# Performance work log

Measured on AMD Instinct MI355X. Metric: run time of the kernel, lower is better.

The kernel has to match this reference:

```python
import jax, jax.numpy as jnp
import numpy as np

N = 6720      # 16 graphs * 420 nodes
E = 33600     # 16 graphs * 2100 edges (5 per node)
DIN = 2048
H1, C1 = 2, 1024   # conv1: heads=2, out=1024 -> concat 2048
H2, C2 = 1, 64     # conv2: heads=1, out=64
ED = 64            # edge_dim
NODES_PER_GRAPH = 420


def _lin(k, fi, fo):
    return jax.random.normal(k, (fi, fo), jnp.float32) / np.sqrt(fi).astype(np.float32)


def setup_inputs() -> dict:
    key = jax.random.key(0)
    ks = jax.random.split(key, 24)
    d = {}
    d["x"] = jax.random.normal(ks[0], (N, DIN), jnp.float32)
    d["edge_index"] = jax.random.randint(ks[1], (2, E), 0, N)
    # tiled learned edge_features param (torch.rand init), one 2100xED block per graph
    ef = jax.random.uniform(ks[2], (5 * NODES_PER_GRAPH, ED), jnp.float32)
    d["edge_attr"] = jnp.tile(ef, (N // NODES_PER_GRAPH, 1))
    HC1 = H1 * C1
    d["q1_w"] = _lin(ks[3], DIN, HC1); d["q1_b"] = jax.random.normal(ks[4], (HC1,)) * 0.01
    d["k1_w"] = _lin(ks[5], DIN, HC1); d["k1_b"] = jax.random.normal(ks[6], (HC1,)) * 0.01
    d["v1_w"] = _lin(ks[7], DIN, HC1); d["v1_b"] = jax.random.normal(ks[8], (HC1,)) * 0.01
    d["e1_w"] = _lin(ks[9], ED, HC1)                      # lin_edge has no bias in PyG
    d["s1_w"] = _lin(ks[10], DIN, HC1); d["s1_b"] = jax.random.normal(ks[11], (HC1,)) * 0.01
    HC2 = H2 * C2
    d["q2_w"] = _lin(ks[12], HC1, HC2); d["q2_b"] = jax.random.normal(ks[13], (HC2,)) * 0.01
    d["k2_w"] = _lin(ks[14], HC1, HC2); d["k2_b"] = jax.random.normal(ks[15], (HC2,)) * 0.01
    d["v2_w"] = _lin(ks[16], HC1, HC2); d["v2_b"] = jax.random.normal(ks[17], (HC2,)) * 0.01
    d["e2_w"] = _lin(ks[18], ED, HC2)
    d["s2_w"] = _lin(ks[19], HC1, HC2); d["s2_b"] = jax.random.normal(ks[20], (HC2,)) * 0.01
    return d


def _transformer_conv(x, src, dst, edge_attr, qw, qb, kw, kb, vw, vb, ew, sw, sb, H, C):
    """PyG TransformerConv (concat=True, beta=False, root_weight=True)."""
    n = x.shape[0]
    q = (x @ qw + qb).reshape(n, H, C)
    k = (x @ kw + kb).reshape(n, H, C)
    v = (x @ vw + vb).reshape(n, H, C)
    e = (edge_attr @ ew).reshape(-1, H, C)         # [E,H,C]
    kj = k[src] + e                                # gather source keys + edge emb
    alpha = jnp.sum(q[dst] * kj, axis=-1) / np.sqrt(C).astype(np.float32)  # [E,H]
    # scatter-softmax over incoming edges of each target node
    amax = jax.ops.segment_max(alpha, dst, num_segments=n)   # [N,H]
    ex = jnp.exp(alpha - amax[dst])
    denom = jax.ops.segment_sum(ex, dst, num_segments=n)
    attn = ex / (denom[dst] + 1e-16)               # [E,H]
    msg = (v[src] + e) * attn[..., None]           # [E,H,C]
    out = jax.ops.segment_sum(msg, dst, num_segments=n).reshape(n, H * C)
    return out + x @ sw + sb                       # root/skip connection


def reference(x, edge_index, edge_attr,
              q1_w, q1_b, k1_w, k1_b, v1_w, v1_b, e1_w, s1_w, s1_b,
              q2_w, q2_b, k2_w, k2_b, v2_w, v2_b, e2_w, s2_w, s2_b):
    src, dst = edge_index[0], edge_index[1]
    h = jax.nn.relu(_transformer_conv(x, src, dst, edge_attr,
                                      q1_w, q1_b, k1_w, k1_b, v1_w, v1_b,
                                      e1_w, s1_w, s1_b, H1, C1))
    h = jax.nn.relu(_transformer_conv(h, src, dst, edge_attr,
                                      q2_w, q2_b, k2_w, k2_b, v2_w, v2_b,
                                      e2_w, s2_w, s2_b, H2, C2))
    return h.reshape(-1, NODES_PER_GRAPH * 64)     # forward returns here (fc layers are dead code)
```

## Files before the change

### kernel.cpp

```cpp
#include <hip/hip_runtime.h>
#include <hip/hip_bf16.h>
#include <cstdint>
#include <cstddef>

#define NN    6720
#define MPAD  6912
#define NE    33600
#define KDIM  2048
#define HC1   2048
#define EAP   2100

typedef __attribute__((ext_vector_type(8))) short bhalf8;
typedef __attribute__((ext_vector_type(4))) short bhalf4;
typedef __attribute__((ext_vector_type(4))) float fx4;

__device__ __forceinline__ float bf2f(short s) {
    union { unsigned int u; float f; } c;
    c.u = ((unsigned int)(unsigned short)s) << 16;
    return c.f;
}

__device__ __forceinline__ void gload16(const __hip_bfloat16* g, void* lds)
{
    __builtin_amdgcn_global_load_lds(
        (const __attribute__((address_space(1))) unsigned int*)g,
        (__attribute__((address_space(3))) unsigned int*)lds,
        16, 0, 0);
}

#define CFENCE asm volatile("" ::: "memory")

__global__ __launch_bounds__(256, 2) void gemm256x128_fused(
    const __hip_bfloat16* __restrict__ A,
    const __hip_bfloat16* __restrict__ Bt,
    const float* __restrict__ bcat,
    __hip_bfloat16* __restrict__ oq,
    __hip_bfloat16* __restrict__ ok,
    __hip_bfloat16* __restrict__ ov,
    __hip_bfloat16* __restrict__ oh)
{
    __shared__ alignas(16) char Lds[73728];

    const int bid = blockIdx.x;
    const int i0  = bid >> 3;
    const int bx  = (bid & 7) * 8 + (i0 & 7);
    const int by  = i0 >> 3;

    const int tid  = threadIdx.x;
    const int w    = tid >> 6;
    const int lane = tid & 63;
    const int wm = w >> 1, wn = w & 1;
    const int rowA = by * 256;
    const int rowB = bx * 128;

    const int sug = ((lane & 3) ^ ((lane >> 3) & 3)) << 3;
    const __hip_bfloat16* Ag0 = A  + (size_t)(rowA + w * 64 + (lane >> 2)) * KDIM + sug;
    const __hip_bfloat16* Bg0 = Bt + (size_t)(rowB + w * 32 + (lane >> 2)) * KDIM + sug;

    const int rds = (((lane >> 4) ^ (((lane & 15) >> 1) & 3)) << 4);

    fx4 acc[8][4] = {};

#define STAGE(T)                                                          \
    { const int s_ = (T) % 3; const int k0_ = (T) * 32;                   \
      char* ab_ = Lds + s_ * 16384 + w * 4096;                            \
      char* bb_ = Lds + 49152 + s_ * 8192 + w * 2048;                     \
      gload16(Ag0 + k0_, ab_);                                            \
      gload16(Ag0 + k0_ + 16 * KDIM, ab_ + 1024);                         \
      gload16(Ag0 + k0_ + 32 * KDIM, ab_ + 2048);                         \
      gload16(Ag0 + k0_ + 48 * KDIM, ab_ + 3072);                         \
      gload16(Bg0 + k0_, bb_);                                            \
      gload16(Bg0 + k0_ + 16 * KDIM, bb_ + 1024); }

#define TILE(T, VM, DOSTAGE)                                              \
    { if (DOSTAGE) { STAGE((T) + 2); }                                    \
      asm volatile("s_waitcnt vmcnt(" VM ")" ::: "memory");               \
      __builtin_amdgcn_s_barrier(); CFENCE;                               \
      const int s_ = (T) % 3;                                             \
      const char* ap_ = Lds + s_ * 16384;                                 \
      const char* bp_ = Lds + 49152 + s_ * 8192;                          \
      bhalf8 af_[8], bf_[4];                                              \
      _Pragma("unroll")                                                   \
      for (int nj = 0; nj < 4; ++nj)                                      \
          bf_[nj] = *(const bhalf8*)(bp_ + (wn * 64 + nj * 16 + (lane & 15)) * 64 + rds); \
      _Pragma("unroll")                                                   \
      for (int mi = 0; mi < 8; ++mi)                                      \
          af_[mi] = *(const bhalf8*)(ap_ + (wm * 128 + mi * 16 + (lane & 15)) * 64 + rds); \
      __builtin_amdgcn_s_setprio(1);                                      \
      _Pragma("unroll")                                                   \
      for (int mi = 0; mi < 8; ++mi)                                      \
          _Pragma("unroll")                                               \
          for (int nj = 0; nj < 4; ++nj)                                  \
              acc[mi][nj] = __builtin_amdgcn_mfma_f32_16x16x32_bf16(      \
                  af_[mi], bf_[nj], acc[mi][nj], 0, 0, 0);                \
      __builtin_amdgcn_s_setprio(0); CFENCE;                              \
      __builtin_amdgcn_s_barrier(); CFENCE; }

    STAGE(0); STAGE(1);
    for (int t = 0; t < (KDIM / 32) - 2; ++t) {
        TILE(t, "12", 1);
    }
    TILE((KDIM / 32) - 2, "6", 0);
    TILE((KDIM / 32) - 1, "0", 0);

#undef TILE
#undef STAGE

    const int gcol = rowB + wn * 64;
    const int seg  = gcol >> 11;
    const int lcol = gcol & 2047;
    float bv[4];
    #pragma unroll
    for (int nj = 0; nj < 4; ++nj) bv[nj] = bcat[gcol + nj * 16 + (lane & 15)];
    char* scr = Lds + w * 8704;
    const int growA = rowA + wm * 128;
    __hip_bfloat16* dst = (seg == 0) ? oq : (seg == 1) ? ok : (seg == 2) ? ov : oh;

    #pragma unroll
    for (int c = 0; c < 4; ++c) {
        #pragma unroll
        for (int m2 = 0; m2 < 2; ++m2) {
            const int mi = c * 2 + m2;
            #pragma unroll
            for (int nj = 0; nj < 4; ++nj) {
                const int cl = nj * 16 + (lane & 15);
                #pragma unroll
                for (int i2 = 0; i2 < 4; ++i2) {
                    const int rl = m2 * 16 + ((lane >> 4) << 2) + i2;
                    *(float*)(scr + rl * 272 + cl * 4) = acc[mi][nj][i2] + bv[nj];
                }
            }
        }
        asm volatile("s_waitcnt lgkmcnt(0)" ::: "memory");
        CFENCE;
        const int rrow = (lane >> 4);
        const int u    = lane & 15;
        #pragma unroll
        for (int p = 0; p < 8; ++p) {
            const int row = p * 4 + rrow;
            const float4 f = *(const float4*)(scr + row * 272 + u * 16);
            bhalf4 tb;
            tb[0] = (short)__bfloat16_as_ushort(__float2bfloat16(f.x));
            tb[1] = (short)__bfloat16_as_ushort(__float2bfloat16(f.y));
            tb[2] = (short)__bfloat16_as_ushort(__float2bfloat16(f.z));
            tb[3] = (short)__bfloat16_as_ushort(__float2bfloat16(f.w));
            *(bhalf4*)&dst[(size_t)(growA + c * 32 + row) * 2048 + lcol + u * 4] = tb;
        }
        asm volatile("s_waitcnt lgkmcnt(0)" ::: "memory");
        CFENCE;
    }
}

__global__ __launch_bounds__(256) void gemm_bf16(
    const __hip_bfloat16* __restrict__ A,
    const __hip_bfloat16* __restrict__ Bt,
    const float* __restrict__ bias,
    float* __restrict__ C,
    __hip_bfloat16* __restrict__ Cb,
    int M, int N, int K, int flags)
{
    __shared__ alignas(16) __hip_bfloat16 Asm[128 * 64];
    __shared__ alignas(16) __hip_bfloat16 Bsm[128 * 64];
    const int tid  = threadIdx.x;
    const int w    = tid >> 6;
    const int lane = tid & 63;
    const int wr = w >> 1, wc = w & 1;
    const int rowA = blockIdx.y * 128;
    const int rowB = blockIdx.x * 128;
    const int klen = K / gridDim.z;
    const int kbeg = blockIdx.z * klen;

    const int srow = w * 32 + (lane >> 3);
    const int ug8  = ((lane & 7) ^ (lane >> 3)) << 3;
    const __hip_bfloat16* Ag = A  + (size_t)(rowA + srow) * K + ug8;
    const __hip_bfloat16* Bg = Bt + (size_t)(rowB + srow) * K + ug8;
    char* AsBase = (char*)Asm + w * 4096;
    char* BsBase = (char*)Bsm + w * 4096;

    fx4 acc[4][4] = {};

    const int fra = wr * 64 + (lane & 15);
    const int frb = wc * 64 + (lane & 15);
    const int kb  = (lane >> 4) << 4;
    const int swz = (lane & 7) << 4;

    for (int k0 = kbeg; k0 < kbeg + klen; k0 += 64) {
        __syncthreads();
        #pragma unroll
        for (int j = 0; j < 4; ++j) {
            gload16(Ag + (size_t)j * 8 * K + k0, AsBase + j * 1024);
            gload16(Bg + (size_t)j * 8 * K + k0, BsBase + j * 1024);
        }
        __syncthreads();
        #pragma unroll
        for (int kk = 0; kk < 2; ++kk) {
            const int cb = kk * 64 + kb;
            bhalf8 af[4], bfr[4];
            #pragma unroll
            for (int mi = 0; mi < 4; ++mi)
                af[mi] = *(const bhalf8*)((const char*)Asm + (fra + mi * 16) * 128 + (cb ^ swz));
            #pragma unroll
            for (int nj = 0; nj < 4; ++nj)
                bfr[nj] = *(const bhalf8*)((const char*)Bsm + (frb + nj * 16) * 128 + (cb ^ swz));
            #pragma unroll
            for (int mi = 0; mi < 4; ++mi)
                #pragma unroll
                for (int nj = 0; nj < 4; ++nj)
                    acc[mi][nj] = __builtin_amdgcn_mfma_f32_16x16x32_bf16(
                        af[mi], bfr[nj], acc[mi][nj], 0, 0, 0);
        }
    }

    float* Cz = C ? C + (size_t)blockIdx.z * ((size_t)M * N) : nullptr;
    #pragma unroll
    for (int nj = 0; nj < 4; ++nj) {
        const int ccol = rowB + wc * 64 + nj * 16 + (lane & 15);
        const float bv = (flags & 1) ? bias[ccol] : 0.f;
        #pragma unroll
        for (int mi = 0; mi < 4; ++mi) {
            const int crow0 = rowA + wr * 64 + mi * 16 + ((lane >> 4) << 2);
            #pragma unroll
            for (int i = 0; i < 4; ++i) {
                size_t idx = (size_t)(crow0 + i) * N + ccol;
                float v = acc[mi][nj][i] + bv;
                if (flags & 2)  v += Cz[idx];
                if (flags & 16) v += __bfloat162float(Cb[idx]);
                if (flags & 4)  v = fmaxf(v, 0.f);
                if (Cz && !(flags & 8)) Cz[idx] = v;
                if (Cb) Cb[idx] = __float2bfloat16(v);
            }
        }
    }
}

__global__ void reduce4(const float* __restrict__ parts, size_t stride,
                        const float* __restrict__ bias, int colmask,
                        float* __restrict__ dst, int n)
{
    int i = blockIdx.x * 256 + threadIdx.x;
    if (i >= n) return;
    float v = parts[i] + parts[stride + i] + parts[2 * stride + i] + parts[3 * stride + i];
    if (bias) v += bias[i & colmask];
    dst[i] = v;
}

__global__ __launch_bounds__(256) void gemm_tile(
    const float* __restrict__ A, const float* __restrict__ B,
    const float* __restrict__ bias, float* __restrict__ C,
    int M, int N, int K, int flags)
{
    __shared__ float As[16][68];
    __shared__ float Bs[16][64];
    const int tid = threadIdx.x;
    const int bx = blockIdx.x, by = blockIdx.y;
    const int tx = tid & 15, ty = tid >> 4;
    const int arow = tid >> 2, acol = (tid & 3) << 2;
    const int brow = tid >> 4, bcol = (tid & 15) << 2;
    const float* Ag = A + (size_t)(by * 64 + arow) * K + acol;
    const float* Bg = B + (size_t)brow * N + bx * 64 + bcol;
    float acc[4][4] = {};
    for (int k0 = 0; k0 < K; k0 += 16) {
        const float4 av = *(const float4*)(Ag + k0);
        const float4 bv = *(const float4*)(Bg + (size_t)k0 * N);
        __syncthreads();
        As[acol + 0][arow] = av.x;
        As[acol + 1][arow] = av.y;
        As[acol + 2][arow] = av.z;
        As[acol + 3][arow] = av.w;
        *(float4*)&Bs[brow][bcol] = bv;
        __syncthreads();
        #pragma unroll
        for (int kk = 0; kk < 16; ++kk) {
            const float4 a4 = *(const float4*)&As[kk][ty << 2];
            const float4 b4 = *(const float4*)&Bs[kk][tx << 2];
            const float a[4] = {a4.x, a4.y, a4.z, a4.w};
            const float b[4] = {b4.x, b4.y, b4.z, b4.w};
            #pragma unroll
            for (int i = 0; i < 4; ++i)
                #pragma unroll
                for (int j = 0; j < 4; ++j)
                    acc[i][j] += a[i] * b[j];
        }
    }
    const int crow = by * 64 + (ty << 2);
    const int ccol = bx * 64 + (tx << 2);
    float4 b4 = make_float4(0.f, 0.f, 0.f, 0.f);
    if (flags & 1) b4 = *(const float4*)(bias + ccol);
    #pragma unroll
    for (int i = 0; i < 4; ++i) {
        float* cp = C + (size_t)(crow + i) * N + ccol;
        float4 v;
        v.x = acc[i][0] + b4.x; v.y = acc[i][1] + b4.y;
        v.z = acc[i][2] + b4.z; v.w = acc[i][3] + b4.w;
        if (flags & 2) {
            const float4 o = *(const float4*)cp;
            v.x += o.x; v.y += o.y; v.z += o.z; v.w += o.w;
        }
        *(float4*)cp = v;
    }
}

__global__ void count_deg(const int* __restrict__ ei, int* __restrict__ deg)
{
    int e = blockIdx.x * 256 + threadIdx.x;
    if (e < NE) atomicAdd(&deg[ei[NE + e]], 1);
}

__global__ __launch_bounds__(1024) void scan_kernel(const int* __restrict__ deg,
                                                    int* __restrict__ rowptr)
{
    __shared__ int s[1024];
    const int t = threadIdx.x;
    const int base = t * 7;
    int loc[7];
    int sum = 0;
    #pragma unroll
    for (int i = 0; i < 7; ++i) {
        int idx = base + i;
        int v = (idx < NN) ? deg[idx] : 0;
        loc[i] = v; sum += v;
    }
    s[t] = sum;
    __syncthreads();
    for (int off = 1; off < 1024; off <<= 1) {
        int v = (t >= off) ? s[t - off] : 0;
        __syncthreads();
        s[t] += v;
        __syncthreads();
    }
    int running = s[t] - sum;
    #pragma unroll
    for (int i = 0; i < 7; ++i) {
        int idx = base + i;
        if (idx <= NN) rowptr[idx] = running;
        if (idx < NN) running += loc[i];
    }
}

__global__ void fill_csr(const int* __restrict__ ei, const int* __restrict__ rowptr,
                         int* __restrict__ fillctr, int* __restrict__ elist)
{
    int e = blockIdx.x * 256 + threadIdx.x;
    if (e >= NE) return;
    int d = ei[NE + e];
    int pos = atomicAdd(&fillctr[d], 1);
    elist[rowptr[d] + pos] = e;
}

__global__ void sort_csr(const int* __restrict__ rowptr, int* __restrict__ elist)
{
    int n = blockIdx.x * 256 + threadIdx.x;
    if (n >= NN) return;
    int s0 = rowptr[n], s1 = rowptr[n + 1];
    for (int i = s0 + 1; i < s1; ++i) {
        int v = elist[i];
        int j = i - 1;
        while (j >= s0 && elist[j] > v) { elist[j + 1] = elist[j]; --j; }
        elist[j + 1] = v;
    }
}

__global__ void cvt_pad_bf16(const float* __restrict__ src, __hip_bfloat16* __restrict__ dst,
                             int relu)
{
    size_t i = (size_t)(blockIdx.x * 256 + threadIdx.x) * 4;
    int row = (int)(i >> 11);
    float4 v = make_float4(0.f, 0.f, 0.f, 0.f);
    if (row < NN) v = *(const float4*)&src[i];
    if (relu) {
        v.x = fmaxf(v.x, 0.f); v.y = fmaxf(v.y, 0.f);
        v.z = fmaxf(v.z, 0.f); v.w = fmaxf(v.w, 0.f);
    }
    dst[i + 0] = __float2bfloat16(v.x);
    dst[i + 1] = __float2bfloat16(v.y);
    dst[i + 2] = __float2bfloat16(v.z);
    dst[i + 3] = __float2bfloat16(v.w);
}

__global__ __launch_bounds__(256) void transpose_cvt4(
    const float* __restrict__ W0, const float* __restrict__ W1,
    const float* __restrict__ W2, const float* __restrict__ W3,
    __hip_bfloat16* __restrict__ dst)
{
    const float* W = (blockIdx.z == 0) ? W0 : (blockIdx.z == 1) ? W1
                   : (blockIdx.z == 2) ? W2 : W3;
    __hip_bfloat16* Bt = dst + (size_t)blockIdx.z * KDIM * KDIM;
    __shared__ float t[32][33];
    int kb = blockIdx.y * 32, nb = blockIdx.x * 32;
    int tx = threadIdx.x & 31, ty = threadIdx.x >> 5;
    #pragma unroll
    for (int i = 0; i < 32; i += 8)
        t[ty + i][tx] = W[(size_t)(kb + ty + i) * KDIM + nb + tx];
    __syncthreads();
    #pragma unroll
    for (int i = 0; i < 32; i += 8)
        Bt[(size_t)(nb + ty + i) * KDIM + kb + tx] = __float2bfloat16(t[tx][ty + i]);
}

__global__ void build_misc(
    const float* __restrict__ q1b, const float* __restrict__ k1b,
    const float* __restrict__ v1b, const float* __restrict__ s1b,
    const float* __restrict__ e1w,
    const float* __restrict__ q2w, const float* __restrict__ k2w,
    const float* __restrict__ v2w, const float* __restrict__ s2w,
    const float* __restrict__ q2bb, const float* __restrict__ k2bb,
    const float* __restrict__ v2bb, const float* __restrict__ s2bb,
    float* __restrict__ bcat, __hip_bfloat16* __restrict__ w1pp,
    __hip_bfloat16* __restrict__ w1ppT, __hip_bfloat16* __restrict__ w2t,
    float* __restrict__ b2)
{
    int idx = blockIdx.x * 256 + threadIdx.x;
    if (idx < 8192) {
        int seg = idx >> 11, j = idx & 2047;
        const float* b = (seg == 0) ? q1b : (seg == 1) ? k1b : (seg == 2) ? v1b : s1b;
        bcat[idx] = b[j];
        return;
    }
    idx -= 8192;
    if (idx < 262144) {
        int p = idx >> 11, j = idx & 2047;
        float v = ((j >> 10) == (p >> 6)) ? e1w[(size_t)(p & 63) * KDIM + j] : 0.f;
        w1pp[idx] = __float2bfloat16(v);
        return;
    }
    idx -= 262144;
    if (idx < 262144) {
        int n = idx >> 7, k = idx & 127;
        float v = ((n >> 10) == (k >> 6)) ? e1w[(size_t)(k & 63) * KDIM + n] : 0.f;
        w1ppT[idx] = __float2bfloat16(v);
        return;
    }
    idx -= 262144;
    int c = idx >> 11, d = idx & 2047;
    int g = c >> 6, j = c & 63;
    const float* w = (g == 0) ? q2w : (g == 1) ? k2w : (g == 2) ? v2w : s2w;
    w2t[idx] = __float2bfloat16(w[(size_t)d * 64 + j]);
    if (d == 0) {
        const float* b = (g == 0) ? q2bb : (g == 1) ? k2bb : (g == 2) ? v2bb : s2bb;
        b2[c] = b[j];
    }
}

__global__ __launch_bounds__(256) void node1_kernel(
    const __hip_bfloat16* __restrict__ q1b, const __hip_bfloat16* __restrict__ k1b,
    const __hip_bfloat16* __restrict__ v1b,
    const float* __restrict__ P1, const float* __restrict__ ea,
    const int* __restrict__ ei, const int* __restrict__ rowptr,
    const int* __restrict__ elist,
    __hip_bfloat16* __restrict__ h1, __hip_bfloat16* __restrict__ R1)
{
    __shared__ int   s_src[256];
    __shared__ int   s_em[256];
    __shared__ float s_at[256][2];
    const int n = blockIdx.x;
    const int s0 = rowptr[n];
    const int deg = rowptr[n + 1] - s0;
    const int w = threadIdx.x >> 6, lane = threadIdx.x & 63;

    for (int j = w; j < deg; j += 4) {
        const int e = elist[s0 + j];
        const int src = ei[e];
        const int em = e % EAP;
        if (lane == 0) { s_src[j] = src; s_em[j] = em; }
        const float eaj = ea[(size_t)em * 64 + lane];
        #pragma unroll
        for (int h = 0; h < 2; ++h) {
            const __hip_bfloat16* qh = q1b + (size_t)n * HC1 + h * 1024 + lane * 16;
            const __hip_bfloat16* kh = k1b + (size_t)src * HC1 + h * 1024 + lane * 16;
            bhalf8 qa = *(const bhalf8*)qh, qc = *(const bhalf8*)(qh + 8);
            bhalf8 ka = *(const bhalf8*)kh, kc = *(const bhalf8*)(kh + 8);
            float s = 0.f;
            #pragma unroll
            for (int jj = 0; jj < 8; ++jj) s += bf2f(qa[jj]) * bf2f(ka[jj]);
            #pragma unroll
            for (int jj = 0; jj < 8; ++jj) s += bf2f(qc[jj]) * bf2f(kc[jj]);
            s += eaj * P1[(size_t)n * 128 + h * 64 + lane];
            #pragma unroll
            for (int off = 32; off; off >>= 1) s += __shfl_xor(s, off);
            if (lane == 0) s_at[j][h] = s * 0.03125f;
        }
    }
    __syncthreads();

    if (threadIdx.x < 2) {
        const int h = threadIdx.x;
        float m = -1e30f;
        for (int j = 0; j < deg; ++j) m = fmaxf(m, s_at[j][h]);
        float sum = 0.f;
        for (int j = 0; j < deg; ++j) {
            float ex = __expf(s_at[j][h] - m);
            s_at[j][h] = ex; sum += ex;
        }
        float inv = 1.f / (sum + 1e-16f);
        for (int j = 0; j < deg; ++j) s_at[j][h] *= inv;
    }
    __syncthreads();

    if (threadIdx.x < 128) {
        const int h = threadIdx.x >> 6, jj = threadIdx.x & 63;
        float r = 0.f;
        for (int j = 0; j < deg; ++j)
            r += s_at[j][h] * ea[(size_t)s_em[j] * 64 + jj];
        R1[(size_t)n * 128 + threadIdx.x] = __float2bfloat16(r);
    }

    const int c0 = threadIdx.x * 8;
    const int h = c0 >> 10;
    float acc[8];
    const bhalf8 cur = *(const bhalf8*)&h1[(size_t)n * HC1 + c0];
    #pragma unroll
    for (int jj = 0; jj < 8; ++jj) acc[jj] = bf2f(cur[jj]);
    for (int j = 0; j < deg; ++j) {
        const float at = s_at[j][h];
        bhalf8 v = *(const bhalf8*)&v1b[(size_t)s_src[j] * HC1 + c0];
        #pragma unroll
        for (int jj = 0; jj < 8; ++jj) acc[jj] += at * bf2f(v[jj]);
    }
    bhalf8 o;
    #pragma unroll
    for (int jj = 0; jj < 8; ++jj)
        o[jj] = (short)__bfloat16_as_ushort(__float2bfloat16(acc[jj]));
    *(bhalf8*)&h1[(size_t)n * HC1 + c0] = o;
}

__global__ __launch_bounds__(64) void node2_kernel(
    const float* __restrict__ qkvs2, const float* __restrict__ E2s,
    const int* __restrict__ ei, const int* __restrict__ rowptr,
    const int* __restrict__ elist, float* __restrict__ out)
{
    __shared__ float s_at[256];
    __shared__ int   s_src[256];
    __shared__ int   s_em[256];
    const int n = blockIdx.x;
    const int s0 = rowptr[n];
    const int deg = rowptr[n + 1] - s0;
    const int c = threadIdx.x;
    const float q = qkvs2[(size_t)n * 256 + c];

    for (int j = 0; j < deg; ++j) {
        const int e = elist[s0 + j];
        const int src = ei[e];
        const int em = e % EAP;
        float s = q * (qkvs2[(size_t)src * 256 + 64 + c] + E2s[(size_t)em * 64 + c]);
        #pragma unroll
        for (int off = 32; off; off >>= 1) s += __shfl_xor(s, off);
        if (c == 0) { s_at[j] = s * 0.125f; s_src[j] = src; s_em[j] = em; }
    }
    __syncthreads();
    float m = -1e30f;
    for (int j = 0; j < deg; ++j) m = fmaxf(m, s_at[j]);
    float sum = 0.f;
    for (int j = 0; j < deg; ++j) sum += __expf(s_at[j] - m);
    const float inv = 1.f / (sum + 1e-16f);

    float acc = qkvs2[(size_t)n * 256 + 192 + c];
    for (int j = 0; j < deg; ++j) {
        const float at = __expf(s_at[j] - m) * inv;
        acc += at * (qkvs2[(size_t)s_src[j] * 256 + 128 + c] + E2s[(size_t)s_em[j] * 64 + c]);
    }
    out[(size_t)n * 64 + c] = fmaxf(acc, 0.f);
}

extern "C" void kernel_launch(void* const* d_in, const int* in_sizes, int n_in,
                              void* d_out, int out_size, void* d_ws, size_t ws_size,
                              hipStream_t stream)
{
    const float* x   = (const float*)d_in[0];
    const int*   ei  = (const int*)d_in[1];
    const float* ea  = (const float*)d_in[2];
    const float* q1w = (const float*)d_in[3];
    const float* q1b = (const float*)d_in[4];
    const float* k1w = (const float*)d_in[5];
    const float* k1b = (const float*)d_in[6];
    const float* v1w = (const float*)d_in[7];
    const float* v1b = (const float*)d_in[8];
    const float* e1w = (const float*)d_in[9];
    const float* s1w = (const float*)d_in[10];
    const float* s1b = (const float*)d_in[11];
    const float* q2w = (const float*)d_in[12];
    const float* q2b = (const float*)d_in[13];
    const float* k2w = (const float*)d_in[14];
    const float* k2b = (const float*)d_in[15];
    const float* v2w = (const float*)d_in[16];
    const float* v2b = (const float*)d_in[17];
    const float* e2w = (const float*)d_in[18];
    const float* s2w = (const float*)d_in[19];
    const float* s2b = (const float*)d_in[20];
    float* out = (float*)d_out;

    char* base = (char*)d_ws;
    size_t off = 0;
    auto alloc = [&](size_t nbytes) {
        size_t o = off; off += (nbytes + 255) & ~(size_t)255; return o;
    };
    const size_t xb_off   = alloc((size_t)MPAD * KDIM * 2);
    const size_t wcat_off = alloc((size_t)4 * KDIM * KDIM * 2);
    __hip_bfloat16* xb    = (__hip_bfloat16*)(base + xb_off);
    __hip_bfloat16* wcat  = (__hip_bfloat16*)(base + wcat_off);
    float*          Cpart = (float*)(base + wcat_off);

    __hip_bfloat16* q1bb  = (__hip_bfloat16*)(base + alloc((size_t)MPAD * HC1 * 2));
    __hip_bfloat16* k1bb  = (__hip_bfloat16*)(base + alloc((size_t)MPAD * HC1 * 2));
    __hip_bfloat16* v1bb  = (__hip_bfloat16*)(base + alloc((size_t)MPAD * HC1 * 2));
    __hip_bfloat16* h1bf  = (__hip_bfloat16*)(base + alloc((size_t)MPAD * HC1 * 2));
    float*          bcat  = (float*)(base + alloc((size_t)4 * KDIM * 4));
    float*          P1    = (float*)(base + alloc((size_t)MPAD * 128 * 4));
    __hip_bfloat16* R1b   = (__hip_bfloat16*)(base + alloc((size_t)MPAD * 128 * 2));
    __hip_bfloat16* w1pp  = (__hip_bfloat16*)(base + alloc((size_t)128 * KDIM * 2));
    __hip_bfloat16* w1ppT = (__hip_bfloat16*)(base + alloc((size_t)KDIM * 128 * 2));
    __hip_bfloat16* w2t   = (__hip_bfloat16*)(base + alloc((size_t)256 * KDIM * 2));
    float*          b2    = (float*)(base + alloc(256 * 4));
    float*          qkvs2 = (float*)(base + alloc((size_t)MPAD * 256 * 4));
    float*          E2s   = (float*)(base + alloc((size_t)2112 * 64 * 4));
    int* deg    = (int*)(base + alloc((size_t)NN * 4));
    int* fill   = (int*)(base + alloc((size_t)NN * 4));
    int* rowptr = (int*)(base + alloc((size_t)(NN + 1) * 4));
    int* elist  = (int*)(base + alloc((size_t)NE * 4));

    hipMemsetAsync(deg, 0, sizeof(int) * 2 * NN, stream);
    count_deg<<<(NE + 255) / 256, 256, 0, stream>>>(ei, deg);
    scan_kernel<<<1, 1024, 0, stream>>>(deg, rowptr);
    fill_csr<<<(NE + 255) / 256, 256, 0, stream>>>(ei, rowptr, fill, elist);
    sort_csr<<<(NN + 255) / 256, 256, 0, stream>>>(rowptr, elist);

    const int cvblk = (MPAD * KDIM / 4) / 256;
    cvt_pad_bf16<<<cvblk, 256, 0, stream>>>(x, xb, 0);
    transpose_cvt4<<<dim3(KDIM / 32, KDIM / 32, 4), 256, 0, stream>>>(q1w, k1w, v1w, s1w, wcat);
    build_misc<<<4128, 256, 0, stream>>>(q1b, k1b, v1b, s1b, e1w,
                                         q2w, k2w, v2w, s2w, q2b, k2b, v2b, s2b,
                                         bcat, w1pp, w1ppT, w2t, b2);
    gemm_tile<<<dim3(1, 33), 256, 0, stream>>>(ea, e2w, nullptr, E2s, 2112, 64, 64, 0);

    gemm256x128_fused<<<1728, 256, 0, stream>>>(xb, wcat, bcat, q1bb, k1bb, v1bb, h1bf);

    gemm_bf16<<<dim3(1, MPAD / 128, 4), 256, 0, stream>>>(q1bb, w1pp, nullptr, Cpart, nullptr,
                                                          MPAD, 128, KDIM, 0);
    reduce4<<<(MPAD * 128) / 256, 256, 0, stream>>>(Cpart, (size_t)MPAD * 128, nullptr, 0,
                                                    P1, MPAD * 128);

    node1_kernel<<<NN, 256, 0, stream>>>(q1bb, k1bb, v1bb, P1, ea, ei, rowptr, elist, h1bf, R1b);
    gemm_bf16<<<dim3(HC1 / 128, MPAD / 128), 256, 0, stream>>>(R1b, w1ppT, nullptr, nullptr,
                                                               h1bf, MPAD, HC1, 128, 16 | 4);

    gemm_bf16<<<dim3(2, MPAD / 128, 4), 256, 0, stream>>>(h1bf, w2t, nullptr, Cpart, nullptr,
                                                          MPAD, 256, KDIM, 0);
    reduce4<<<(MPAD * 256) / 256, 256, 0, stream>>>(Cpart, (size_t)MPAD * 256, b2, 255,
                                                    qkvs2, MPAD * 256);

    node2_kernel<<<NN, 64, 0, stream>>>(qkvs2, E2s, ei, rowptr, elist, out);

    (void)in_sizes; (void)n_in; (void)out_size; (void)ws_size;
}
```

Before: 456.6 us.

## Fuse preprocessing kernels into one launch and prefetch neighbor rows in node kernels

Merges the bf16 conversion of x, the weight transpose, the misc weight builds and the small edge GEMM into a single prep_kernel, with each block range dispatching to a different job. This removes several launches and lets the independent jobs overlap. node1_kernel now issues loads of up to eight neighbor V rows and its own skip row before the attention phase so that latency overlaps the score computation. node2_kernel keeps the first eight edges' K, V and edge embeddings in registers and only syncs when the degree exceeds eight. The register arrays add register pressure, and shared arrays in node2 shrink to 192 entries, which assumes a bounded degree.

```diff
diff --git a/kernel.cpp b/kernel.cpp
--- a/kernel.cpp
+++ b/kernel.cpp
@@ -9,6 +9,7 @@
 #define KDIM  2048
 #define HC1   2048
 #define EAP   2100
+#define NPF   8
 
 typedef __attribute__((ext_vector_type(8))) short bhalf8;
 typedef __attribute__((ext_vector_type(4))) short bhalf4;
@@ -244,62 +245,6 @@
     dst[i] = v;
 }
 
-__global__ __launch_bounds__(256) void gemm_tile(
-    const float* __restrict__ A, const float* __restrict__ B,
-    const float* __restrict__ bias, float* __restrict__ C,
-    int M, int N, int K, int flags)
-{
-    __shared__ float As[16][68];
-    __shared__ float Bs[16][64];
-    const int tid = threadIdx.x;
-    const int bx = blockIdx.x, by = blockIdx.y;
-    const int tx = tid & 15, ty = tid >> 4;
-    const int arow = tid >> 2, acol = (tid & 3) << 2;
-    const int brow = tid >> 4, bcol = (tid & 15) << 2;
-    const float* Ag = A + (size_t)(by * 64 + arow) * K + acol;
-    const float* Bg = B + (size_t)brow * N + bx * 64 + bcol;
-    float acc[4][4] = {};
-    for (int k0 = 0; k0 < K; k0 += 16) {
-        const float4 av = *(const float4*)(Ag + k0);
-        const float4 bv = *(const float4*)(Bg + (size_t)k0 * N);
-        __syncthreads();
-        As[acol + 0][arow] = av.x;
-        As[acol + 1][arow] = av.y;
-        As[acol + 2][arow] = av.z;
-        As[acol + 3][arow] = av.w;
-        *(float4*)&Bs[brow][bcol] = bv;
-        __syncthreads();
-        #pragma unroll
-        for (int kk = 0; kk < 16; ++kk) {
-            const float4 a4 = *(const float4*)&As[kk][ty << 2];
-            const float4 b4 = *(const float4*)&Bs[kk][tx << 2];
-            const float a[4] = {a4.x, a4.y, a4.z, a4.w};
-            const float b[4] = {b4.x, b4.y, b4.z, b4.w};
-            #pragma unroll
-            for (int i = 0; i < 4; ++i)
-                #pragma unroll
-                for (int j = 0; j < 4; ++j)
-                    acc[i][j] += a[i] * b[j];
-        }
-    }
-    const int crow = by * 64 + (ty << 2);
-    const int ccol = bx * 64 + (tx << 2);
-    float4 b4 = make_float4(0.f, 0.f, 0.f, 0.f);
-    if (flags & 1) b4 = *(const float4*)(bias + ccol);
-    #pragma unroll
-    for (int i = 0; i < 4; ++i) {
-        float* cp = C + (size_t)(crow + i) * N + ccol;
-        float4 v;
-        v.x = acc[i][0] + b4.x; v.y = acc[i][1] + b4.y;
-        v.z = acc[i][2] + b4.z; v.w = acc[i][3] + b4.w;
-        if (flags & 2) {
-            const float4 o = *(const float4*)cp;
-            v.x += o.x; v.y += o.y; v.z += o.z; v.w += o.w;
-        }
-        *(float4*)cp = v;
-    }
-}
-
 __global__ void count_deg(const int* __restrict__ ei, int* __restrict__ deg)
 {
     int e = blockIdx.x * 256 + threadIdx.x;
@@ -360,44 +305,11 @@
     }
 }
 
-__global__ void cvt_pad_bf16(const float* __restrict__ src, __hip_bfloat16* __restrict__ dst,
-                             int relu)
-{
-    size_t i = (size_t)(blockIdx.x * 256 + threadIdx.x) * 4;
-    int row = (int)(i >> 11);
-    float4 v = make_float4(0.f, 0.f, 0.f, 0.f);
-    if (row < NN) v = *(const float4*)&src[i];
-    if (relu) {
-        v.x = fmaxf(v.x, 0.f); v.y = fmaxf(v.y, 0.f);
-        v.z = fmaxf(v.z, 0.f); v.w = fmaxf(v.w, 0.f);
-    }
-    dst[i + 0] = __float2bfloat16(v.x);
-    dst[i + 1] = __float2bfloat16(v.y);
-    dst[i + 2] = __float2bfloat16(v.z);
-    dst[i + 3] = __float2bfloat16(v.w);
-}
-
-__global__ __launch_bounds__(256) void transpose_cvt4(
-    const float* __restrict__ W0, const float* __restrict__ W1,
-    const float* __restrict__ W2, const float* __restrict__ W3,
-    __hip_bfloat16* __restrict__ dst)
-{
-    const float* W = (blockIdx.z == 0) ? W0 : (blockIdx.z == 1) ? W1
-                   : (blockIdx.z == 2) ? W2 : W3;
-    __hip_bfloat16* Bt = dst + (size_t)blockIdx.z * KDIM * KDIM;
-    __shared__ float t[32][33];
-    int kb = blockIdx.y * 32, nb = blockIdx.x * 32;
-    int tx = threadIdx.x & 31, ty = threadIdx.x >> 5;
-    #pragma unroll
-    for (int i = 0; i < 32; i += 8)
-        t[ty + i][tx] = W[(size_t)(kb + ty + i) * KDIM + nb + tx];
-    __syncthreads();
-    #pragma unroll
-    for (int i = 0; i < 32; i += 8)
-        Bt[(size_t)(nb + ty + i) * KDIM + kb + tx] = __float2bfloat16(t[tx][ty + i]);
-}
-
-__global__ void build_misc(
+__global__ __launch_bounds__(256) void prep_kernel(
+    const float* __restrict__ x, __hip_bfloat16* __restrict__ xb,
+    const float* __restrict__ q1w, const float* __restrict__ k1w,
+    const float* __restrict__ v1w, const float* __restrict__ s1w,
+    __hip_bfloat16* __restrict__ wcat,
     const float* __restrict__ q1b, const float* __restrict__ k1b,
     const float* __restrict__ v1b, const float* __restrict__ s1b,
     const float* __restrict__ e1w,
@@ -407,37 +319,127 @@
     const float* __restrict__ v2bb, const float* __restrict__ s2bb,
     float* __restrict__ bcat, __hip_bfloat16* __restrict__ w1pp,
     __hip_bfloat16* __restrict__ w1ppT, __hip_bfloat16* __restrict__ w2t,
-    float* __restrict__ b2)
-{
-    int idx = blockIdx.x * 256 + threadIdx.x;
-    if (idx < 8192) {
-        int seg = idx >> 11, j = idx & 2047;
-        const float* b = (seg == 0) ? q1b : (seg == 1) ? k1b : (seg == 2) ? v1b : s1b;
-        bcat[idx] = b[j];
+    float* __restrict__ b2,
+    const float* __restrict__ ea, const float* __restrict__ e2w,
+    float* __restrict__ E2s)
+{
+    __shared__ alignas(16) char plds[8448];
+    const int bid = blockIdx.x;
+    const int tid = threadIdx.x;
+
+    if (bid < 6912) {
+        const int row = bid;
+        const size_t base = (size_t)row * KDIM + tid * 8;
+        float4 v0 = make_float4(0.f, 0.f, 0.f, 0.f), v1 = v0;
+        if (row < NN) {
+            v0 = *(const float4*)&x[base];
+            v1 = *(const float4*)&x[base + 4];
+        }
+        bhalf8 o;
+        o[0] = (short)__bfloat16_as_ushort(__float2bfloat16(v0.x));
+        o[1] = (short)__bfloat16_as_ushort(__float2bfloat16(v0.y));
+        o[2] = (short)__bfloat16_as_ushort(__float2bfloat16(v0.z));
+        o[3] = (short)__bfloat16_as_ushort(__float2bfloat16(v0.w));
+        o[4] = (short)__bfloat16_as_ushort(__float2bfloat16(v1.x));
+        o[5] = (short)__bfloat16_as_ushort(__float2bfloat16(v1.y));
+        o[6] = (short)__bfloat16_as_ushort(__float2bfloat16(v1.z));
+        o[7] = (short)__bfloat16_as_ushort(__float2bfloat16(v1.w));
+        *(bhalf8*)&xb[base] = o;
         return;
     }
-    idx -= 8192;
-    if (idx < 262144) {
-        int p = idx >> 11, j = idx & 2047;
-        float v = ((j >> 10) == (p >> 6)) ? e1w[(size_t)(p & 63) * KDIM + j] : 0.f;
-        w1pp[idx] = __float2bfloat16(v);
+    if (bid < 23296) {
+        const int idx = bid - 6912;
+        const int z   = idx >> 12;
+        const int rem = idx & 4095;
+        const int byi = rem >> 6, bxi = rem & 63;
+        const float* W = (z == 0) ? q1w : (z == 1) ? k1w : (z == 2) ? v1w : s1w;
+        __hip_bfloat16* Bt = wcat + (size_t)z * KDIM * KDIM;
+        float (*t)[33] = (float (*)[33])plds;
+        const int kb = byi * 32, nb = bxi * 32;
+        const int tx = tid & 31, ty = tid >> 5;
+        #pragma unroll
+        for (int i = 0; i < 32; i += 8)
+            t[ty + i][tx] = W[(size_t)(kb + ty + i) * KDIM + nb + tx];
+        __syncthreads();
+        #pragma unroll
+        for (int i = 0; i < 32; i += 8)
+            Bt[(size_t)(nb + ty + i) * KDIM + kb + tx] = __float2bfloat16(t[tx][ty + i]);
         return;
     }
-    idx -= 262144;
-    if (idx < 262144) {
-        int n = idx >> 7, k = idx & 127;
-        float v = ((n >> 10) == (k >> 6)) ? e1w[(size_t)(k & 63) * KDIM + n] : 0.f;
-        w1ppT[idx] = __float2bfloat16(v);
+    if (bid < 27424) {
+        int idx = (bid - 23296) * 256 + tid;
+        if (idx < 8192) {
+            int seg = idx >> 11, j = idx & 2047;
+            const float* b = (seg == 0) ? q1b : (seg == 1) ? k1b : (seg == 2) ? v1b : s1b;
+            bcat[idx] = b[j];
+            return;
+        }
+        idx -= 8192;
+        if (idx < 262144) {
+            int p = idx >> 11, j = idx & 2047;
+            float v = ((j >> 10) == (p >> 6)) ? e1w[(size_t)(p & 63) * KDIM + j] : 0.f;
+            w1pp[idx] = __float2bfloat16(v);
+            return;
+        }
+        idx -= 262144;
+        if (idx < 262144) {
+            int n = idx >> 7, k = idx & 127;
+            float v = ((n >> 10) == (k >> 6)) ? e1w[(size_t)(k & 63) * KDIM + n] : 0.f;
+            w1ppT[idx] = __float2bfloat16(v);
+            return;
+        }
+        idx -= 262144;
+        int c = idx >> 11, d = idx & 2047;
+        int g = c >> 6, j = c & 63;
+        const float* w = (g == 0) ? q2w : (g == 1) ? k2w : (g == 2) ? v2w : s2w;
+        w2t[idx] = __float2bfloat16(w[(size_t)d * 64 + j]);
+        if (d == 0) {
+            const float* b = (g == 0) ? q2bb : (g == 1) ? k2bb : (g == 2) ? v2bb : s2bb;
+            b2[c] = b[j];
+        }
         return;
     }
-    idx -= 262144;
-    int c = idx >> 11, d = idx & 2047;
-    int g = c >> 6, j = c & 63;
-    const float* w = (g == 0) ? q2w : (g == 1) ? k2w : (g == 2) ? v2w : s2w;
-    w2t[idx] = __float2bfloat16(w[(size_t)d * 64 + j]);
-    if (d == 0) {
-        const float* b = (g == 0) ? q2bb : (g == 1) ? k2bb : (g == 2) ? v2bb : s2bb;
-        b2[c] = b[j];
+    {
+        const int byi = bid - 27424;
+        float (*As)[68] = (float (*)[68])plds;
+        float (*Bs)[64] = (float (*)[64])(plds + 4352);
+        const int tx = tid & 15, ty = tid >> 4;
+        const int arow = tid >> 2, acol = (tid & 3) << 2;
+        const int brow = tid >> 4, bcol = (tid & 15) << 2;
+        const float* Ag = ea + (size_t)(byi * 64 + arow) * 64 + acol;
+        const float* Bg = e2w + (size_t)brow * 64 + bcol;
+        float acc[4][4] = {};
+        for (int k0 = 0; k0 < 64; k0 += 16) {
+            const float4 av = *(const float4*)(Ag + k0);
+            const float4 bv = *(const float4*)(Bg + (size_t)k0 * 64);
+            __syncthreads();
+            As[acol + 0][arow] = av.x;
+            As[acol + 1][arow] = av.y;
+            As[acol + 2][arow] = av.z;
+            As[acol + 3][arow] = av.w;
+            *(float4*)&Bs[brow][bcol] = bv;
+            __syncthreads();
+            #pragma unroll
+            for (int kk = 0; kk < 16; ++kk) {
+                const float4 a4 = *(const float4*)&As[kk][ty << 2];
+                const float4 b4 = *(const float4*)&Bs[kk][tx << 2];
+                const float a[4] = {a4.x, a4.y, a4.z, a4.w};
+                const float b[4] = {b4.x, b4.y, b4.z, b4.w};
+                #pragma unroll
+                for (int i = 0; i < 4; ++i)
+                    #pragma unroll
+                    for (int j = 0; j < 4; ++j)
+                        acc[i][j] += a[i] * b[j];
+            }
+        }
+        const int crow = byi * 64 + (ty << 2);
+        const int ccol = (tx << 2);
+        #pragma unroll
+        for (int i = 0; i < 4; ++i) {
+            float4 v;
+            v.x = acc[i][0]; v.y = acc[i][1]; v.z = acc[i][2]; v.w = acc[i][3];
+            *(float4*)&E2s[(size_t)(crow + i) * 64 + ccol] = v;
+        }
     }
 }
 
@@ -456,6 +458,17 @@
     const int s0 = rowptr[n];
     const int deg = rowptr[n + 1] - s0;
     const int w = threadIdx.x >> 6, lane = threadIdx.x & 63;
+    const int c0 = threadIdx.x * 8;
+    const int h = c0 >> 10;
+
+    const int dpf = (deg < NPF) ? deg : NPF;
+    bhalf8 vpre[NPF];
+    for (int j = 0; j < dpf; ++j) {
+        const int e = elist[s0 + j];
+        const int src = ei[e];
+        vpre[j] = *(const bhalf8*)&v1b[(size_t)src * HC1 + c0];
+    }
+    const bhalf8 cur = *(const bhalf8*)&h1[(size_t)n * HC1 + c0];
 
     for (int j = w; j < deg; j += 4) {
         const int e = elist[s0 + j];
@@ -464,9 +477,9 @@
         if (lane == 0) { s_src[j] = src; s_em[j] = em; }
         const float eaj = ea[(size_t)em * 64 + lane];
         #pragma unroll
-        for (int h = 0; h < 2; ++h) {
-            const __hip_bfloat16* qh = q1b + (size_t)n * HC1 + h * 1024 + lane * 16;
-            const __hip_bfloat16* kh = k1b + (size_t)src * HC1 + h * 1024 + lane * 16;
+        for (int hh = 0; hh < 2; ++hh) {
+            const __hip_bfloat16* qh = q1b + (size_t)n * HC1 + hh * 1024 + lane * 16;
+            const __hip_bfloat16* kh = k1b + (size_t)src * HC1 + hh * 1024 + lane * 16;
             bhalf8 qa = *(const bhalf8*)qh, qc = *(const bhalf8*)(qh + 8);
             bhalf8 ka = *(const bhalf8*)kh, kc = *(const bhalf8*)(kh + 8);
             float s = 0.f;
@@ -474,43 +487,45 @@
             for (int jj = 0; jj < 8; ++jj) s += bf2f(qa[jj]) * bf2f(ka[jj]);
             #pragma unroll
             for (int jj = 0; jj < 8; ++jj) s += bf2f(qc[jj]) * bf2f(kc[jj]);
-            s += eaj * P1[(size_t)n * 128 + h * 64 + lane];
+            s += eaj * P1[(size_t)n * 128 + hh * 64 + lane];
             #pragma unroll
             for (int off = 32; off; off >>= 1) s += __shfl_xor(s, off);
-            if (lane == 0) s_at[j][h] = s * 0.03125f;
+            if (lane == 0) s_at[j][hh] = s * 0.03125f;
         }
     }
     __syncthreads();
 
     if (threadIdx.x < 2) {
-        const int h = threadIdx.x;
+        const int hh = threadIdx.x;
         float m = -1e30f;
-        for (int j = 0; j < deg; ++j) m = fmaxf(m, s_at[j][h]);
+        for (int j = 0; j < deg; ++j) m = fmaxf(m, s_at[j][hh]);
         float sum = 0.f;
         for (int j = 0; j < deg; ++j) {
-            float ex = __expf(s_at[j][h] - m);
-            s_at[j][h] = ex; sum += ex;
+            float ex = __expf(s_at[j][hh] - m);
+            s_at[j][hh] = ex; sum += ex;
         }
         float inv = 1.f / (sum + 1e-16f);
-        for (int j = 0; j < deg; ++j) s_at[j][h] *= inv;
+        for (int j = 0; j < deg; ++j) s_at[j][hh] *= inv;
     }
     __syncthreads();
 
     if (threadIdx.x < 128) {
-        const int h = threadIdx.x >> 6, jj = threadIdx.x & 63;
+        const int hh = threadIdx.x >> 6, jj = threadIdx.x & 63;
         float r = 0.f;
         for (int j = 0; j < deg; ++j)
-            r += s_at[j][h] * ea[(size_t)s_em[j] * 64 + jj];
+            r += s_at[j][hh] * ea[(size_t)s_em[j] * 64 + jj];
         R1[(size_t)n * 128 + threadIdx.x] = __float2bfloat16(r);
     }
 
-    const int c0 = threadIdx.x * 8;
-    const int h = c0 >> 10;
     float acc[8];
-    const bhalf8 cur = *(const bhalf8*)&h1[(size_t)n * HC1 + c0];
     #pragma unroll
     for (int jj = 0; jj < 8; ++jj) acc[jj] = bf2f(cur[jj]);
-    for (int j = 0; j < deg; ++j) {
+    for (int j = 0; j < dpf; ++j) {
+        const float at = s_at[j][h];
+        #pragma unroll
+        for (int jj = 0; jj < 8; ++jj) acc[jj] += at * bf2f(vpre[j][jj]);
+    }
+    for (int j = NPF; j < deg; ++j) {
         const float at = s_at[j][h];
         bhalf8 v = *(const bhalf8*)&v1b[(size_t)s_src[j] * HC1 + c0];
         #pragma unroll
@@ -528,35 +543,58 @@
     const int* __restrict__ ei, const int* __restrict__ rowptr,
     const int* __restrict__ elist, float* __restrict__ out)
 {
-    __shared__ float s_at[256];
-    __shared__ int   s_src[256];
-    __shared__ int   s_em[256];
+    __shared__ float s_at[192];
+    __shared__ int   s_src[192];
+    __shared__ int   s_em[192];
     const int n = blockIdx.x;
     const int s0 = rowptr[n];
     const int deg = rowptr[n + 1] - s0;
     const int c = threadIdx.x;
     const float q = qkvs2[(size_t)n * 256 + c];
 
-    for (int j = 0; j < deg; ++j) {
+    const int dpf = (deg < NPF) ? deg : NPF;
+    int   srcj[NPF], emj[NPF];
+    float kj[NPF], e2j[NPF], vj[NPF];
+    for (int j = 0; j < dpf; ++j) {
+        const int e = elist[s0 + j];
+        srcj[j] = ei[e];
+        emj[j]  = e % EAP;
+        kj[j]   = qkvs2[(size_t)srcj[j] * 256 + 64 + c];
+        e2j[j]  = E2s[(size_t)emj[j] * 64 + c];
+        vj[j]   = qkvs2[(size_t)srcj[j] * 256 + 128 + c];
+    }
+    float at[NPF];
+    for (int j = 0; j < dpf; ++j) {
+        float s = q * (kj[j] + e2j[j]);
+        #pragma unroll
+        for (int off = 32; off; off >>= 1) s += __shfl_xor(s, off);
+        at[j] = s * 0.125f;
+    }
+    for (int j = NPF; j < deg; ++j) {
         const int e = elist[s0 + j];
         const int src = ei[e];
         const int em = e % EAP;
         float s = q * (qkvs2[(size_t)src * 256 + 64 + c] + E2s[(size_t)em * 64 + c]);
         #pragma unroll
         for (int off = 32; off; off >>= 1) s += __shfl_xor(s, off);
-        if (c == 0) { s_at[j] = s * 0.125f; s_src[j] = src; s_em[j] = em; }
-    }
-    __syncthreads();
+        if (c == 0) { s_at[j - NPF] = s * 0.125f; s_src[j - NPF] = src; s_em[j - NPF] = em; }
+    }
+    if (deg > NPF) __syncthreads();
+
     float m = -1e30f;
-    for (int j = 0; j < deg; ++j) m = fmaxf(m, s_at[j]);
+    for (int j = 0; j < dpf; ++j) m = fmaxf(m, at[j]);
+    for (int j = NPF; j < deg; ++j) m = fmaxf(m, s_at[j - NPF]);
     float sum = 0.f;
-    for (int j = 0; j < deg; ++j) sum += __expf(s_at[j] - m);
+    for (int j = 0; j < dpf; ++j) sum += __expf(at[j] - m);
+    for (int j = NPF; j < deg; ++j) sum += __expf(s_at[j - NPF] - m);
     const float inv = 1.f / (sum + 1e-16f);
 
     float acc = qkvs2[(size_t)n * 256 + 192 + c];
-    for (int j = 0; j < deg; ++j) {
-        const float at = __expf(s_at[j] - m) * inv;
-        acc += at * (qkvs2[(size_t)s_src[j] * 256 + 128 + c] + E2s[(size_t)s_em[j] * 64 + c]);
+    for (int j = 0; j < dpf; ++j)
+        acc += (__expf(at[j] - m) * inv) * (vj[j] + e2j[j]);
+    for (int j = NPF; j < deg; ++j) {
+        const float a = __expf(s_at[j - NPF] - m) * inv;
+        acc += a * (qkvs2[(size_t)s_src[j - NPF] * 256 + 128 + c] + E2s[(size_t)s_em[j - NPF] * 64 + c]);
     }
     out[(size_t)n * 64 + c] = fmaxf(acc, 0.f);
 }
@@ -623,13 +661,11 @@
     fill_csr<<<(NE + 255) / 256, 256, 0, stream>>>(ei, rowptr, fill, elist);
     sort_csr<<<(NN + 255) / 256, 256, 0, stream>>>(rowptr, elist);
 
-    const int cvblk = (MPAD * KDIM / 4) / 256;
-    cvt_pad_bf16<<<cvblk, 256, 0, stream>>>(x, xb, 0);
-    transpose_cvt4<<<dim3(KDIM / 32, KDIM / 32, 4), 256, 0, stream>>>(q1w, k1w, v1w, s1w, wcat);
-    build_misc<<<4128, 256, 0, stream>>>(q1b, k1b, v1b, s1b, e1w,
-                                         q2w, k2w, v2w, s2w, q2b, k2b, v2b, s2b,
-                                         bcat, w1pp, w1ppT, w2t, b2);
-    gemm_tile<<<dim3(1, 33), 256, 0, stream>>>(ea, e2w, nullptr, E2s, 2112, 64, 64, 0);
+    prep_kernel<<<27457, 256, 0, stream>>>(
+        x, xb, q1w, k1w, v1w, s1w, wcat,
+        q1b, k1b, v1b, s1b, e1w,
+        q2w, k2w, v2w, s2w, q2b, k2b, v2b, s2b,
+        bcat, w1pp, w1ppT, w2t, b2, ea, e2w, E2s);
 
     gemm256x128_fused<<<1728, 256, 0, stream>>>(xb, wcat, bcat, q1bb, k1bb, v1bb, h1bf);
 
```

Result: slower. 1.389 ms (+204.3%).
